# Optimization experiments

Hardware: AMD Instinct MI355X
Metric: run time of the kernel (lower is better)

The kernel has to match this reference:

```python
import jax, jax.numpy as jnp
import numpy as np

B, S, D, H = 4, 2048, 1024, 16
HD = D // H


def setup_inputs() -> dict:
    key = jax.random.key(0)
    ks = jax.random.split(key, 12)
    scale = 1.0 / np.sqrt(D)
    inp = {
        "query": jax.random.normal(ks[0], (B, S, D), jnp.float32),
        "key_": jax.random.normal(ks[1], (B, S, D), jnp.float32),
        "value": jax.random.normal(ks[2], (B, S, D), jnp.float32),
        "Wq": jax.random.normal(ks[3], (D, D), jnp.float32) * scale,
        "bq": jnp.zeros((D,), jnp.float32),
        "Wk": jax.random.normal(ks[4], (D, D), jnp.float32) * scale,
        "bk": jnp.zeros((D,), jnp.float32),
        "Wv": jax.random.normal(ks[5], (D, D), jnp.float32) * scale,
        "bv": jnp.zeros((D,), jnp.float32),
        "Wo": jax.random.normal(ks[6], (D, D), jnp.float32) * scale,
        "bo": jnp.zeros((D,), jnp.float32),
        # causal mask: 1 where attention allowed, 0 where masked (masked_fill(mask==0, -inf))
        "mask": jnp.tril(jnp.ones((S, S), jnp.int32))[None, None, :, :],
    }
    return inp


def reference(query, key_, value, Wq, bq, Wk, bk, Wv, bv, Wo, bo, mask):
    def split_heads(x):  # [B,S,D] -> [B,H,S,HD]
        return x.reshape(B, S, H, HD).transpose(0, 2, 1, 3)

    Q = split_heads(query @ Wq.T + bq)
    K = split_heads(key_ @ Wk.T + bk)
    V = split_heads(value @ Wv.T + bv)

    scores = jnp.einsum("bhqd,bhkd->bhqk", Q, K) / np.sqrt(HD).astype(np.float32)
    scores = jnp.where(mask == 0, -jnp.inf, scores)
    attn = jax.nn.softmax(scores, axis=-1)  # [B,H,S,S]
    out = jnp.einsum("bhqk,bhkd->bhqd", attn, V)  # [B,H,S,HD]
    concat = out.transpose(0, 2, 1, 3).reshape(B, S, D)
    return concat @ Wo.T + bo
```

## Files before the change

kernel.cpp:

```cpp
#include <hip/hip_runtime.h>
#include <hip/hip_bf16.h>
#include <math.h>

#define BB 4
#define SS 2048
#define DD 1024
#define HH 16
#define HD 64

#define NEG_BIG (-1e30f)


typedef short v8s __attribute__((ext_vector_type(8)));
typedef float v4f __attribute__((ext_vector_type(4)));

__device__ inline unsigned cvt_pk_bf16(float lo, float hi) {
    unsigned r;
    asm("v_cvt_pk_bf16_f32 %0, %1, %2" : "=v"(r) : "v"(lo), "v"(hi));
    return r;
}

__device__ inline short f2bf(float f) {
    return (short)cvt_pk_bf16(f, f);
}

__device__ inline v4f v4f_zero() {
    v4f z;
    z[0] = 0.f; z[1] = 0.f; z[2] = 0.f; z[3] = 0.f;
    return z;
}

__device__ inline v8s cvt8(v4f a, v4f b) {
    union { unsigned u[4]; v8s s; } x;
    x.u[0] = cvt_pk_bf16(a[0], a[1]);
    x.u[1] = cvt_pk_bf16(a[2], a[3]);
    x.u[2] = cvt_pk_bf16(b[0], b[1]);
    x.u[3] = cvt_pk_bf16(b[2], b[3]);
    return x.s;
}

__device__ inline v8s load8f(const float* p) {
    return cvt8(*(const v4f*)p, *(const v4f*)(p + 4));
}

__device__ inline void gll16(const void* g, void* l) {
    __builtin_amdgcn_global_load_lds(
        (const __attribute__((address_space(1))) unsigned*)g,
        (__attribute__((address_space(3))) unsigned*)l, 16, 0, 0);
}

__global__ __launch_bounds__(256) void conv_bf16_kernel(
    const float* __restrict__ in, short* __restrict__ out, int n8) {
    int i = blockIdx.x * 256 + threadIdx.x;
    const int stride = gridDim.x * 256;
    for (; i < n8; i += stride) {
        *((v8s*)out + i) = load8f(in + (size_t)i * 8);
    }
}

template <int MODE>
__global__ __launch_bounds__(256) void gemm_kernel(
    const void* __restrict__ Av, const void* __restrict__ Bv,
    const float* __restrict__ bias, void* __restrict__ Cv) {
    __shared__ short sA[128 * 32];
    __shared__ short sB[128 * 32];

    const int tid = threadIdx.x;
    const int lane = tid & 63;
    const int wave = tid >> 6;
    const int quad = lane >> 4;
    const int l16 = lane & 15;
    const int wm = wave >> 1;
    const int wn = wave & 1;

    int bx, by;
    if (MODE != 1) {
        int b = blockIdx.x + (blockIdx.y << 3);
        int l = ((b & 7) << 6) + (b >> 3);
        bx = l & 7;
        by = l >> 3;
    } else {
        bx = blockIdx.x;
        by = blockIdx.y;
    }
    const int m0 = by * 128;
    const int n0 = bx * 128;

    const int grow = (wave << 5) + (lane >> 2);
    const int gcol = (lane & 3) << 3;
    const int ldoff = wave << 10;

    const short* As = (const short*)Av;
    size_t gaA0, gaA1;
    if (MODE == 3) {
        int ma = m0 + grow, mb = m0 + grow + 16;
        gaA0 = ((size_t)((ma >> 11) * HH) * SS + (ma & 2047)) * HD;
        gaA1 = ((size_t)((mb >> 11) * HH) * SS + (mb & 2047)) * HD;
    } else {
        gaA0 = (size_t)(m0 + grow) * 1024 + gcol;
        gaA1 = gaA0 + (size_t)16 * 1024;
    }

    const short* Bs = (const short*)Bv;
    const float* Bf = (const float*)Bv;
    size_t gaB0 = 0, gaB1 = 0;
    if (MODE != 1) {
        gaB0 = (size_t)(n0 + grow) * 1024 + gcol;
        gaB1 = gaB0 + (size_t)16 * 1024;
    }
    const int idx0 = tid << 3, idx1 = (256 + tid) << 3;
    const float* Bsrc0 = (MODE == 1)
        ? Bf + (size_t)(n0 + (idx0 >> 5)) * 1024 + (idx0 & 31) : nullptr;
    const float* Bsrc1 = (MODE == 1)
        ? Bf + (size_t)(n0 + (idx1 >> 5)) * 1024 + (idx1 & 31) : nullptr;

    v4f acc[4][4];
#pragma unroll
    for (int i = 0; i < 4; i++)
#pragma unroll
        for (int j = 0; j < 4; j++) acc[i][j] = v4f_zero();

    for (int k0 = 0; k0 < 1024; k0 += 32) {
        __syncthreads();
        if (MODE == 3) {
            size_t hoff = (size_t)(k0 >> 6) * (SS * HD) + (k0 & 63) + gcol;
            gll16(As + gaA0 + hoff, sA + ldoff);
            gll16(As + gaA1 + hoff, sA + ldoff + 512);
        } else {
            gll16(As + gaA0 + k0, sA + ldoff);
            gll16(As + gaA1 + k0, sA + ldoff + 512);
        }
        if (MODE == 1) {
            *(v8s*)&sB[idx0] = load8f(Bsrc0 + k0);
            *(v8s*)&sB[idx1] = load8f(Bsrc1 + k0);
        } else {
            gll16(Bs + gaB0 + k0, sB + ldoff);
            gll16(Bs + gaB1 + k0, sB + ldoff + 512);
        }
        __syncthreads();

        v8s af[4], bfr[4];
#pragma unroll
        for (int i = 0; i < 4; i++)
            af[i] = *(const v8s*)&sA[(wm * 64 + i * 16 + l16) * 32 + quad * 8];
#pragma unroll
        for (int j = 0; j < 4; j++)
            bfr[j] = *(const v8s*)&sB[(wn * 64 + j * 16 + l16) * 32 + quad * 8];
#pragma unroll
        for (int i = 0; i < 4; i++)
#pragma unroll
            for (int j = 0; j < 4; j++)
                acc[i][j] = __builtin_amdgcn_mfma_f32_16x16x32_bf16(
                    af[i], bfr[j], acc[i][j], 0, 0, 0);
    }

#pragma unroll
    for (int i = 0; i < 4; i++) {
#pragma unroll
        for (int j = 0; j < 4; j++) {
#pragma unroll
            for (int r = 0; r < 4; r++) {
                int ml = wm * 64 + i * 16 + quad * 4 + r;
                int nl = wn * 64 + j * 16 + l16;
                int m = m0 + ml;
                int n = n0 + nl;
                float v = acc[i][j][r];
                if (MODE == 0) {
                    v += bias[n];
                    int b = m >> 11, s = m & 2047, h = n >> 6, d = n & 63;
                    ((short*)Cv)[(((size_t)(b * HH + h) * SS + s) << 6) + d] =
                        f2bf(v);
                } else if (MODE == 1) {
                    v += bias[m];
                    int h = m >> 6, d = m & 63, b = n >> 11, s = n & 2047;
                    ((short*)Cv)[((size_t)(b * HH + h) * HD + d) * SS + s] =
                        f2bf(v);
                } else {
                    v += bias[n];
                    ((float*)Cv)[(size_t)m * 1024 + n] = v;
                }
            }
        }
    }
}

__global__ __launch_bounds__(256) void attn_kernel(
    short* __restrict__ QO, const short* __restrict__ Kt,
    const short* __restrict__ Vt) {
    constexpr int LDR = 64 + 8;
    __shared__ short sK[64 * 64];
    __shared__ short sV[64 * 64];
    __shared__ short sP[4][16 * LDR];

    const int tid = threadIdx.x;
    const int lane = tid & 63;
    const int wave = tid >> 6;
    const int quad = lane >> 4;
    const int l16 = lane & 15;
    const int qt = (int)gridDim.x - 1 - (int)blockIdx.x;
    const int bh = blockIdx.y;

    short* Qh = QO + (size_t)bh * SS * HD;
    const short* Kh = Kt + (size_t)bh * SS * HD;
    const short* Vh = Vt + (size_t)bh * HD * SS;

    const int qrow = qt * 64 + wave * 16 + l16;
    v8s qf[2];
    qf[0] = *(const v8s*)&Qh[(size_t)qrow * HD + quad * 8];
    qf[1] = *(const v8s*)&Qh[(size_t)qrow * HD + 32 + quad * 8];

    v8s onesb;
#pragma unroll
    for (int i = 0; i < 8; i++) onesb[i] = (short)0x3F80;

    v4f o[4];
#pragma unroll
    for (int j = 0; j < 4; j++) o[j] = v4f_zero();
    v4f oSum = v4f_zero();
    float mOld[4];
#pragma unroll
    for (int r = 0; r < 4; r++) mOld[r] = NEG_BIG;

    const int qg_base = qt * 64 + wave * 16 + quad * 4;

    const int rc0 = (quad * 8) ^ ((l16 & 7) << 3);
    const int rc1 = (32 + quad * 8) ^ ((l16 & 7) << 3);

    for (int kt = 0; kt <= qt; kt++) {
        __syncthreads();
#pragma unroll
        for (int p = 0; p < 2; p++) {
            int idx = (p * 256 + tid) * 8;
            int r = idx >> 6;
            int c = idx & 63;
            int cs = c ^ ((r & 7) << 3);
            *(v8s*)&sK[r * 64 + cs] =
                *(const v8s*)&Kh[(size_t)(kt * 64 + r) * HD + c];
            *(v8s*)&sV[r * 64 + cs] =
                *(const v8s*)&Vh[(size_t)r * SS + kt * 64 + c];
        }
        __syncthreads();

        __builtin_amdgcn_s_setprio(1);
        v4f sc[4];
#pragma unroll
        for (int j = 0; j < 4; j++) {
            v8s b0 = *(const v8s*)&sK[(j * 16 + l16) * 64 + rc0];
            v8s b1 = *(const v8s*)&sK[(j * 16 + l16) * 64 + rc1];
            v4f t = __builtin_amdgcn_mfma_f32_16x16x32_bf16(qf[0], b0,
                                                            v4f_zero(), 0, 0, 0);
            sc[j] = __builtin_amdgcn_mfma_f32_16x16x32_bf16(qf[1], b1, t, 0, 0, 0);
        }
        __builtin_amdgcn_s_setprio(0);

        float x[4][4];
        const bool diag = (kt == qt);
#pragma unroll
        for (int j = 0; j < 4; j++) {
#pragma unroll
            for (int r = 0; r < 4; r++) {
                float v = sc[j][r] * 0.125f;
                if (diag) {
                    int kg = kt * 64 + j * 16 + l16;
                    int qg = qg_base + r;
                    if (kg > qg) v = NEG_BIG;
                }
                x[j][r] = v;
            }
        }

        float mNew[4], alpha[4];
#pragma unroll
        for (int r = 0; r < 4; r++) {
            float t = fmaxf(fmaxf(x[0][r], x[1][r]), fmaxf(x[2][r], x[3][r]));
#pragma unroll
            for (int off = 8; off >= 1; off >>= 1) t = fmaxf(t, __shfl_xor(t, off));
            mNew[r] = fmaxf(mOld[r], t);
            alpha[r] = __expf(mOld[r] - mNew[r]);
            mOld[r] = mNew[r];
        }

        short* Pw = sP[wave];
#pragma unroll
        for (int j = 0; j < 4; j++)
#pragma unroll
            for (int r = 0; r < 4; r++) {
                float p = __expf(x[j][r] - mNew[r]);
                Pw[(quad * 4 + r) * LDR + j * 16 + l16] = f2bf(p);
            }
#pragma unroll
        for (int j = 0; j < 4; j++)
#pragma unroll
            for (int r = 0; r < 4; r++) o[j][r] *= alpha[r];
#pragma unroll
        for (int r = 0; r < 4; r++) oSum[r] *= alpha[r];

        v8s pa0 = *(const v8s*)&Pw[l16 * LDR + quad * 8];
        v8s pa1 = *(const v8s*)&Pw[l16 * LDR + 32 + quad * 8];
        __builtin_amdgcn_s_setprio(1);
#pragma unroll
        for (int j = 0; j < 4; j++) {
            v8s v0 = *(const v8s*)&sV[(j * 16 + l16) * 64 + rc0];
            v8s v1 = *(const v8s*)&sV[(j * 16 + l16) * 64 + rc1];
            o[j] = __builtin_amdgcn_mfma_f32_16x16x32_bf16(pa0, v0, o[j], 0, 0, 0);
            o[j] = __builtin_amdgcn_mfma_f32_16x16x32_bf16(pa1, v1, o[j], 0, 0, 0);
        }
        oSum = __builtin_amdgcn_mfma_f32_16x16x32_bf16(pa0, onesb, oSum, 0, 0, 0);
        oSum = __builtin_amdgcn_mfma_f32_16x16x32_bf16(pa1, onesb, oSum, 0, 0, 0);
        __builtin_amdgcn_s_setprio(0);
    }

#pragma unroll
    for (int r = 0; r < 4; r++) {
        float inv = 1.f / oSum[r];
        int s = qg_base + r;
#pragma unroll
        for (int j = 0; j < 4; j++) {
            float v = o[j][r] * inv;
            Qh[(size_t)s * HD + j * 16 + l16] = f2bf(v);
        }
    }
}

extern "C" void kernel_launch(void* const* d_in, const int* in_sizes, int n_in,
                              void* d_out, int out_size, void* d_ws, size_t ws_size,
                              hipStream_t stream) {
    const float* query = (const float*)d_in[0];
    const float* key_ = (const float*)d_in[1];
    const float* value = (const float*)d_in[2];
    const float* Wq = (const float*)d_in[3];
    const float* bq = (const float*)d_in[4];
    const float* Wk = (const float*)d_in[5];
    const float* bk = (const float*)d_in[6];
    const float* Wv = (const float*)d_in[7];
    const float* bv = (const float*)d_in[8];
    const float* Wo = (const float*)d_in[9];
    const float* bo = (const float*)d_in[10];
    float* out = (float*)d_out;

    const size_t NE = (size_t)BB * SS * DD;
    const size_t WE = (size_t)DD * DD;

    short* qx  = (short*)d_out;
    short* kx  = (short*)d_out + NE;
    short* wqb = (short*)d_ws + NE;
    short* wkb = (short*)d_out;
    short* wvb = (short*)d_out + WE;
    short* vw  = (short*)d_out + NE;
    short* qw  = (short*)d_ws;
    short* kw  = (short*)d_ws + NE;
    short* wob = (short*)d_ws + NE;

    dim3 blk(256);
    const int n8a = (int)(NE / 8);
    const int n8w = (int)(WE / 8);

    conv_bf16_kernel<<<dim3(2048), blk, 0, stream>>>(query, qx, n8a);
    conv_bf16_kernel<<<dim3(2048), blk, 0, stream>>>(key_, kx, n8a);
    conv_bf16_kernel<<<dim3(512), blk, 0, stream>>>(Wq, wqb, n8w);
    gemm_kernel<0><<<dim3(8, 64), blk, 0, stream>>>(qx, wqb, bq, qw);
    conv_bf16_kernel<<<dim3(512), blk, 0, stream>>>(Wk, wkb, n8w);
    gemm_kernel<0><<<dim3(8, 64), blk, 0, stream>>>(kx, wkb, bk, kw);
    conv_bf16_kernel<<<dim3(512), blk, 0, stream>>>(Wv, wvb, n8w);
    gemm_kernel<1><<<dim3(64, 8), blk, 0, stream>>>(wvb, value, bv, vw);
    attn_kernel<<<dim3(SS / 64, BB * HH), blk, 0, stream>>>(qw, kw, vw);
    conv_bf16_kernel<<<dim3(512), blk, 0, stream>>>(Wo, wob, n8w);
    gemm_kernel<3><<<dim3(8, 64), blk, 0, stream>>>(qw, wob, bo, out);
}
```

Before: 464.0 us.

## Fuse Q/K/V projections into one launch with in-kernel fp32-to-bf16 activation conversion

Replaces the separate activation conversion kernels and three projection GEMM launches with a single grid-z-indexed kernel. It reads fp32 activations directly and converts them to bf16 while staging into LDS. This removes two full-activation conversion passes, their extra global traffic, and two launches. In exchange, the activation load becomes a synchronous register path rather than a direct global-to-LDS load, and the V projection now writes its transposed layout with a strided scatter.

```diff
diff --git a/kernel.cpp b/kernel.cpp
--- a/kernel.cpp
+++ b/kernel.cpp
@@ -58,10 +58,13 @@
     }
 }
 
-template <int MODE>
-__global__ __launch_bounds__(256) void gemm_kernel(
-    const void* __restrict__ Av, const void* __restrict__ Bv,
-    const float* __restrict__ bias, void* __restrict__ Cv) {
+__global__ __launch_bounds__(256) void fused_qkv_kernel(
+    const float* __restrict__ actq, const float* __restrict__ actk,
+    const float* __restrict__ actv, const short* __restrict__ wqp,
+    const short* __restrict__ wkp, const short* __restrict__ wvp,
+    const float* __restrict__ bqp, const float* __restrict__ bkp,
+    const float* __restrict__ bvp, short* __restrict__ cq,
+    short* __restrict__ ck, short* __restrict__ cv) {
     __shared__ short sA[128 * 32];
     __shared__ short sB[128 * 32];
 
@@ -72,47 +75,29 @@
     const int l16 = lane & 15;
     const int wm = wave >> 1;
     const int wn = wave & 1;
-
-    int bx, by;
-    if (MODE != 1) {
-        int b = blockIdx.x + (blockIdx.y << 3);
-        int l = ((b & 7) << 6) + (b >> 3);
-        bx = l & 7;
-        by = l >> 3;
-    } else {
-        bx = blockIdx.x;
-        by = blockIdx.y;
-    }
+    const int z = blockIdx.z;
+
+    const float* act = (z == 0) ? actq : (z == 1) ? actk : actv;
+    const short* W = (z == 0) ? wqp : (z == 1) ? wkp : wvp;
+    const float* bias = (z == 0) ? bqp : (z == 1) ? bkp : bvp;
+    short* Cv = (z == 0) ? cq : (z == 1) ? ck : cv;
+
+    int b = blockIdx.x + (blockIdx.y << 3);
+    int l = ((b & 7) << 6) + (b >> 3);
+    const int bx = l & 7;
+    const int by = l >> 3;
     const int m0 = by * 128;
     const int n0 = bx * 128;
 
     const int grow = (wave << 5) + (lane >> 2);
     const int gcol = (lane & 3) << 3;
     const int ldoff = wave << 10;
-
-    const short* As = (const short*)Av;
-    size_t gaA0, gaA1;
-    if (MODE == 3) {
-        int ma = m0 + grow, mb = m0 + grow + 16;
-        gaA0 = ((size_t)((ma >> 11) * HH) * SS + (ma & 2047)) * HD;
-        gaA1 = ((size_t)((mb >> 11) * HH) * SS + (mb & 2047)) * HD;
-    } else {
-        gaA0 = (size_t)(m0 + grow) * 1024 + gcol;
-        gaA1 = gaA0 + (size_t)16 * 1024;
-    }
-
-    const short* Bs = (const short*)Bv;
-    const float* Bf = (const float*)Bv;
-    size_t gaB0 = 0, gaB1 = 0;
-    if (MODE != 1) {
-        gaB0 = (size_t)(n0 + grow) * 1024 + gcol;
-        gaB1 = gaB0 + (size_t)16 * 1024;
-    }
+    const size_t gaB0 = (size_t)(n0 + grow) * 1024 + gcol;
+    const size_t gaB1 = gaB0 + (size_t)16 * 1024;
+
     const int idx0 = tid << 3, idx1 = (256 + tid) << 3;
-    const float* Bsrc0 = (MODE == 1)
-        ? Bf + (size_t)(n0 + (idx0 >> 5)) * 1024 + (idx0 & 31) : nullptr;
-    const float* Bsrc1 = (MODE == 1)
-        ? Bf + (size_t)(n0 + (idx1 >> 5)) * 1024 + (idx1 & 31) : nullptr;
+    const float* Asrc0 = act + (size_t)(m0 + (idx0 >> 5)) * 1024 + (idx0 & 31);
+    const float* Asrc1 = act + (size_t)(m0 + (idx1 >> 5)) * 1024 + (idx1 & 31);
 
     v4f acc[4][4];
 #pragma unroll
@@ -122,21 +107,10 @@
 
     for (int k0 = 0; k0 < 1024; k0 += 32) {
         __syncthreads();
-        if (MODE == 3) {
-            size_t hoff = (size_t)(k0 >> 6) * (SS * HD) + (k0 & 63) + gcol;
-            gll16(As + gaA0 + hoff, sA + ldoff);
-            gll16(As + gaA1 + hoff, sA + ldoff + 512);
-        } else {
-            gll16(As + gaA0 + k0, sA + ldoff);
-            gll16(As + gaA1 + k0, sA + ldoff + 512);
-        }
-        if (MODE == 1) {
-            *(v8s*)&sB[idx0] = load8f(Bsrc0 + k0);
-            *(v8s*)&sB[idx1] = load8f(Bsrc1 + k0);
-        } else {
-            gll16(Bs + gaB0 + k0, sB + ldoff);
-            gll16(Bs + gaB1 + k0, sB + ldoff + 512);
-        }
+        gll16(W + gaB0 + k0, sB + ldoff);
+        gll16(W + gaB1 + k0, sB + ldoff + 512);
+        *(v8s*)&sA[idx0] = load8f(Asrc0 + k0);
+        *(v8s*)&sA[idx1] = load8f(Asrc1 + k0);
         __syncthreads();
 
         v8s af[4], bfr[4];
@@ -164,21 +138,93 @@
                 int nl = wn * 64 + j * 16 + l16;
                 int m = m0 + ml;
                 int n = n0 + nl;
-                float v = acc[i][j][r];
-                if (MODE == 0) {
-                    v += bias[n];
-                    int b = m >> 11, s = m & 2047, h = n >> 6, d = n & 63;
-                    ((short*)Cv)[(((size_t)(b * HH + h) * SS + s) << 6) + d] =
-                        f2bf(v);
-                } else if (MODE == 1) {
-                    v += bias[m];
-                    int h = m >> 6, d = m & 63, b = n >> 11, s = n & 2047;
-                    ((short*)Cv)[((size_t)(b * HH + h) * HD + d) * SS + s] =
-                        f2bf(v);
+                float v = acc[i][j][r] + bias[n];
+                int bb = m >> 11, s = m & 2047, h = n >> 6, d = n & 63;
+                if (z < 2) {
+                    Cv[(((size_t)(bb * HH + h) * SS + s) << 6) + d] = f2bf(v);
                 } else {
-                    v += bias[n];
-                    ((float*)Cv)[(size_t)m * 1024 + n] = v;
+                    Cv[((size_t)(bb * HH + h) * HD + d) * SS + s] = f2bf(v);
                 }
+            }
+        }
+    }
+}
+
+__global__ __launch_bounds__(256) void gemm_out_kernel(
+    const void* __restrict__ Av, const void* __restrict__ Bv,
+    const float* __restrict__ bias, void* __restrict__ Cv) {
+    __shared__ short sA[128 * 32];
+    __shared__ short sB[128 * 32];
+
+    const int tid = threadIdx.x;
+    const int lane = tid & 63;
+    const int wave = tid >> 6;
+    const int quad = lane >> 4;
+    const int l16 = lane & 15;
+    const int wm = wave >> 1;
+    const int wn = wave & 1;
+
+    int b = blockIdx.x + (blockIdx.y << 3);
+    int l = ((b & 7) << 6) + (b >> 3);
+    const int bx = l & 7;
+    const int by = l >> 3;
+    const int m0 = by * 128;
+    const int n0 = bx * 128;
+
+    const int grow = (wave << 5) + (lane >> 2);
+    const int gcol = (lane & 3) << 3;
+    const int ldoff = wave << 10;
+
+    const short* As = (const short*)Av;
+    int ma = m0 + grow, mb = m0 + grow + 16;
+    const size_t gaA0 = ((size_t)((ma >> 11) * HH) * SS + (ma & 2047)) * HD;
+    const size_t gaA1 = ((size_t)((mb >> 11) * HH) * SS + (mb & 2047)) * HD;
+
+    const short* Bs = (const short*)Bv;
+    const size_t gaB0 = (size_t)(n0 + grow) * 1024 + gcol;
+    const size_t gaB1 = gaB0 + (size_t)16 * 1024;
+
+    v4f acc[4][4];
+#pragma unroll
+    for (int i = 0; i < 4; i++)
+#pragma unroll
+        for (int j = 0; j < 4; j++) acc[i][j] = v4f_zero();
+
+    for (int k0 = 0; k0 < 1024; k0 += 32) {
+        __syncthreads();
+        size_t hoff = (size_t)(k0 >> 6) * (SS * HD) + (k0 & 63) + gcol;
+        gll16(As + gaA0 + hoff, sA + ldoff);
+        gll16(As + gaA1 + hoff, sA + ldoff + 512);
+        gll16(Bs + gaB0 + k0, sB + ldoff);
+        gll16(Bs + gaB1 + k0, sB + ldoff + 512);
+        __syncthreads();
+
+        v8s af[4], bfr[4];
+#pragma unroll
+        for (int i = 0; i < 4; i++)
+            af[i] = *(const v8s*)&sA[(wm * 64 + i * 16 + l16) * 32 + quad * 8];
+#pragma unroll
+        for (int j = 0; j < 4; j++)
+            bfr[j] = *(const v8s*)&sB[(wn * 64 + j * 16 + l16) * 32 + quad * 8];
+#pragma unroll
+        for (int i = 0; i < 4; i++)
+#pragma unroll
+            for (int j = 0; j < 4; j++)
+                acc[i][j] = __builtin_amdgcn_mfma_f32_16x16x32_bf16(
+                    af[i], bfr[j], acc[i][j], 0, 0, 0);
+    }
+
+#pragma unroll
+    for (int i = 0; i < 4; i++) {
+#pragma unroll
+        for (int j = 0; j < 4; j++) {
+#pragma unroll
+            for (int r = 0; r < 4; r++) {
+                int ml = wm * 64 + i * 16 + quad * 4 + r;
+                int nl = wn * 64 + j * 16 + l16;
+                int m = m0 + ml;
+                int n = n0 + nl;
+                ((float*)Cv)[(size_t)m * 1024 + n] = acc[i][j][r] + bias[n];
             }
         }
     }
@@ -341,29 +387,23 @@
     const size_t NE = (size_t)BB * SS * DD;
     const size_t WE = (size_t)DD * DD;
 
-    short* qx  = (short*)d_out;
-    short* kx  = (short*)d_out + NE;
-    short* wqb = (short*)d_ws + NE;
-    short* wkb = (short*)d_out;
-    short* wvb = (short*)d_out + WE;
-    short* vw  = (short*)d_out + NE;
+    short* wqb = (short*)d_out;
+    short* wkb = (short*)d_out + WE;
+    short* wvb = (short*)d_out + 2 * WE;
     short* qw  = (short*)d_ws;
     short* kw  = (short*)d_ws + NE;
+    short* vw  = (short*)d_out + NE;
     short* wob = (short*)d_ws + NE;
 
     dim3 blk(256);
-    const int n8a = (int)(NE / 8);
     const int n8w = (int)(WE / 8);
 
-    conv_bf16_kernel<<<dim3(2048), blk, 0, stream>>>(query, qx, n8a);
-    conv_bf16_kernel<<<dim3(2048), blk, 0, stream>>>(key_, kx, n8a);
     conv_bf16_kernel<<<dim3(512), blk, 0, stream>>>(Wq, wqb, n8w);
-    gemm_kernel<0><<<dim3(8, 64), blk, 0, stream>>>(qx, wqb, bq, qw);
     conv_bf16_kernel<<<dim3(512), blk, 0, stream>>>(Wk, wkb, n8w);
-    gemm_kernel<0><<<dim3(8, 64), blk, 0, stream>>>(kx, wkb, bk, kw);
     conv_bf16_kernel<<<dim3(512), blk, 0, stream>>>(Wv, wvb, n8w);
-    gemm_kernel<1><<<dim3(64, 8), blk, 0, stream>>>(wvb, value, bv, vw);
+    fused_qkv_kernel<<<dim3(8, 64, 3), blk, 0, stream>>>(
+        query, key_, value, wqb, wkb, wvb, bq, bk, bv, qw, kw, vw);
     attn_kernel<<<dim3(SS / 64, BB * HH), blk, 0, stream>>>(qw, kw, vw);
     conv_bf16_kernel<<<dim3(512), blk, 0, stream>>>(Wo, wob, n8w);
-    gemm_kernel<3><<<dim3(8, 64), blk, 0, stream>>>(qw, wob, bo, out);
-}
+    gemm_out_kernel<<<dim3(8, 64), blk, 0, stream>>>(qw, wob, bo, out);
+}
```

New measurement: 477.1 us. 2.8% more time.
